# Optimization experiments

Measured on AMD Instinct MI355X. Metric: run time of the kernel, lower is better.

## Reference

```python
import jax, jax.numpy as jnp
import numpy as np

NUM_NODES = 100000
EMB = 64
HID = 128
OUT = 64
N_EDGES = 1600000
N_LABEL = 200000


def setup_inputs() -> dict:
    key = jax.random.key(0)
    ks = jax.random.split(key, 8)
    return {
        "emb": jax.random.normal(ks[0], (NUM_NODES, EMB), jnp.float32) * 0.05,
        "w1l": jax.random.normal(ks[1], (HID, EMB), jnp.float32) * 0.05,
        "w1r": jax.random.normal(ks[2], (HID, EMB), jnp.float32) * 0.05,
        "b1": jnp.zeros((HID,), jnp.float32),
        "w2l": jax.random.normal(ks[3], (OUT, HID), jnp.float32) * 0.05,
        "w2r": jax.random.normal(ks[4], (OUT, HID), jnp.float32) * 0.05,
        "b2": jnp.zeros((OUT,), jnp.float32),
        "edge_index": jax.random.randint(ks[5], (2, N_EDGES), 0, NUM_NODES, jnp.int32),
        "edge_label_index": jax.random.randint(ks[6], (2, N_LABEL), 0, NUM_NODES, jnp.int32),
    }


def reference(emb, w1l, w1r, b1, w2l, w2r, b2, edge_index, edge_label_index):
    # PyG SAGEConv (aggr='mean'): out = mean_{j in N(i)} x_j @ W_l^T + b_l + x_i @ W_r^T
    n = emb.shape[0]
    src, dst = edge_index[0], edge_index[1]
    # in-degree per destination node, clamped to avoid div-by-zero (isolated nodes -> 0 agg)
    deg = jax.ops.segment_sum(jnp.ones(src.shape, emb.dtype), dst, num_segments=n)
    inv_deg = 1.0 / jnp.maximum(deg, 1.0)

    def sage(x, wl, wr, b):
        agg = jax.ops.segment_sum(x[src], dst, num_segments=n) * inv_deg[:, None]
        return agg @ wl.T + x @ wr.T + b

    h = jax.nn.relu(sage(emb, w1l, w1r, b1))  # dropout is identity in eval mode
    z = sage(h, w2l, w2r, b2)  # [N, OUT]
    # dot-product decode over candidate pairs
    return jnp.sum(z[edge_label_index[0]] * z[edge_label_index[1]], axis=-1)
```

## Files before the change

kernel.cpp:

```cpp
#include <hip/hip_runtime.h>

#define NN   100000
#define EMB  64
#define HID  128
#define OUTD 64
#define NE   1600000
#define NL   200000
#define NBUK 782
#define CAPT 2560

#define BIN_BLOCKS  160
#define TILE        10240
#define CEMB_BLOCKS 400
#define CW_BLOCKS   32

typedef __attribute__((ext_vector_type(4))) float f32x4;
typedef __attribute__((ext_vector_type(8))) short s16x8;
typedef __attribute__((ext_vector_type(4))) unsigned short us4;
typedef __attribute__((ext_vector_type(8))) unsigned short us8;

__device__ __forceinline__ unsigned short f2bf(float f) {
    unsigned u = __float_as_uint(f);
    u += 0x7FFFu + ((u >> 16) & 1u);
    return (unsigned short)(u >> 16);
}
__device__ __forceinline__ float bf2f(unsigned short h) {
    return __uint_as_float(((unsigned)h) << 16);
}

__global__ void __launch_bounds__(512) prep_kernel(
        const int* __restrict__ src, const int* __restrict__ dst,
        int* __restrict__ gcur, int* __restrict__ tmp,
        const float* __restrict__ emb, unsigned short* __restrict__ embb,
        const float* __restrict__ w1l, const float* __restrict__ w1r,
        const float* __restrict__ w2l, const float* __restrict__ w2r,
        unsigned short* __restrict__ w1cat, unsigned short* __restrict__ w2cat) {
    const int bid = blockIdx.x;
    const int tid = threadIdx.x;

    if (bid < BIN_BLOCKS) {
        __shared__ int hist[NBUK];
        __shared__ int base[NBUK];
        const int t0  = bid * TILE;
        const int end = min(t0 + TILE, NE);

        for (int k = tid; k < NBUK; k += 512) hist[k] = 0;
        __syncthreads();

        for (int i = t0 + tid; i < end; i += 512)
            atomicAdd(&hist[__builtin_nontemporal_load(dst + i) >> 7], 1);
        __syncthreads();

        for (int k = tid; k < NBUK; k += 512) {
            int c = hist[k];
            base[k] = c ? atomicAdd(&gcur[k], c) : 0;
        }
        __syncthreads();

        for (int i = t0 + tid; i < end; i += 512) {
            int d = __builtin_nontemporal_load(dst + i);
            int s = __builtin_nontemporal_load(src + i);
            int b = d >> 7;
            int pos = atomicAdd(&base[b], 1);
            if (pos < CAPT) tmp[b * CAPT + pos] = ((d & 127) << 17) | s;
        }
    } else if (bid < BIN_BLOCKS + CEMB_BLOCKS) {
        for (int i = (bid - BIN_BLOCKS) * 512 + tid; i < NN * 16; i += CEMB_BLOCKS * 512) {
            float4 v = ((const float4*)emb)[i];
            us4 o;
            o.x = f2bf(v.x); o.y = f2bf(v.y); o.z = f2bf(v.z); o.w = f2bf(v.w);
            ((us4*)embb)[i] = o;
        }
    } else {
        int t = (bid - BIN_BLOCKS - CEMB_BLOCKS) * 512 + tid;
        if (t >= 128 * 128) return;
        int o = t >> 7, k = t & 127;
        w1cat[t] = f2bf(k < 64 ? w1l[o * 64 + k] : w1r[o * 64 + (k - 64)]);
        w2cat[t] = f2bf(o < 64 ? w2l[o * 128 + k] : w2r[(o - 64) * 128 + k]);
    }
}

template<bool L1>
__global__ void __launch_bounds__(512) agg_kernel(
        const int* __restrict__ gcur, const int* __restrict__ tmp,
        const unsigned short* __restrict__ xb,
        const unsigned short* __restrict__ hzb, const float* __restrict__ bias,
        unsigned short* __restrict__ outb) {
    __shared__ int scnt[128];
    __shared__ int soff[128];
    __shared__ int scur[128];
    __shared__ int slist[CAPT];

    const int b    = blockIdx.x;
    const int tid  = threadIdx.x;
    const int lane = tid & 63;
    const int wv   = tid >> 6;

    if (tid < 128) scnt[tid] = 0;
    __syncthreads();

    const int cnt = min(gcur[b], CAPT);
    const int* tb = tmp + b * CAPT;

    for (int i = tid; i < cnt; i += 512)
        atomicAdd(&scnt[tb[i] >> 17], 1);
    __syncthreads();

    if (tid == 0) {
        int acc = 0;
        for (int r = 0; r < 128; ++r) {
            soff[r] = acc;
            scur[r] = acc;
            acc += scnt[r];
        }
    }
    __syncthreads();

    for (int i = tid; i < cnt; i += 512) {
        int p = tb[i];
        int pos = atomicAdd(&scur[p >> 17], 1);
        slist[pos] = p & 0x1FFFF;
    }
    __syncthreads();

    const float bb = L1 ? 0.f : bias[lane];

#define LDX(c) bf2f(xb[(size_t)(c) * 64 + lane])
    for (int r = wv; r < 128; r += 8) {
        const int node = b * 128 + r;
        if (node >= NN) continue;
        const int s = soff[r];
        const int d = scnt[r];
        float acc = 0.f;
        int j = 0;
        for (; j + 8 <= d; j += 8) {
            int c0 = slist[s + j + 0], c1 = slist[s + j + 1];
            int c2 = slist[s + j + 2], c3 = slist[s + j + 3];
            int c4 = slist[s + j + 4], c5 = slist[s + j + 5];
            int c6 = slist[s + j + 6], c7 = slist[s + j + 7];
            float v0 = LDX(c0), v1 = LDX(c1), v2 = LDX(c2), v3 = LDX(c3);
            float v4 = LDX(c4), v5 = LDX(c5), v6 = LDX(c6), v7 = LDX(c7);
            acc += ((v0 + v1) + (v2 + v3)) + ((v4 + v5) + (v6 + v7));
        }
        if (j + 4 <= d) {
            int c0 = slist[s + j + 0], c1 = slist[s + j + 1];
            int c2 = slist[s + j + 2], c3 = slist[s + j + 3];
            float v0 = LDX(c0), v1 = LDX(c1), v2 = LDX(c2), v3 = LDX(c3);
            acc += (v0 + v1) + (v2 + v3);
            j += 4;
        }
        for (; j < d; ++j) acc += LDX(slist[s + j]);

        const float inv = 1.0f / fmaxf((float)d, 1.0f);
        if (L1) {
            outb[(size_t)node * 64 + lane] = f2bf(acc * inv);
        } else {
            outb[(size_t)node * 64 + lane] =
                f2bf(acc * inv + bf2f(hzb[(size_t)node * 64 + lane]) + bb);
        }
    }
#undef LDX
}

__global__ void __launch_bounds__(512) gemm_mfma_kernel(
        const unsigned short* __restrict__ aggb, const unsigned short* __restrict__ embb,
        const unsigned short* __restrict__ w1cat, const float* __restrict__ b1,
        const unsigned short* __restrict__ w2cat,
        unsigned short* __restrict__ p2b, unsigned short* __restrict__ hzb) {
    __shared__ unsigned short h_lds[128 * 136];

    const int tid  = threadIdx.x;
    const int lane = tid & 63;
    const int w    = tid >> 6;
    const int l15  = lane & 15;
    const int lk   = lane >> 4;
    const int n_base = blockIdx.x * 128;
    const int mrow0  = w * 16;

    f32x4 acc[8];
#pragma unroll
    for (int nt = 0; nt < 8; ++nt) acc[nt] = (f32x4)(0.f);

    s16x8 a[4];
    {
        const int n = n_base + mrow0 + l15;
        const bool ok = n < NN;
#pragma unroll
        for (int ks = 0; ks < 4; ++ks) {
            const int kc = ks * 32 + lk * 8;
            a[ks] = (s16x8)(short)0;
            if (ok) {
                const unsigned short* ap = (kc < 64)
                    ? (aggb + (size_t)n * 64 + kc)
                    : (embb + (size_t)n * 64 + (kc - 64));
                a[ks] = *(const s16x8*)ap;
            }
        }
    }
#pragma unroll
    for (int ks = 0; ks < 4; ++ks) {
        const int kc = ks * 32 + lk * 8;
#pragma unroll
        for (int nt = 0; nt < 8; ++nt) {
            s16x8 bv = *(const s16x8*)(w1cat + (nt * 16 + l15) * 128 + kc);
            acc[nt] = __builtin_amdgcn_mfma_f32_16x16x32_bf16(a[ks], bv, acc[nt], 0, 0, 0);
        }
    }

    float b1v[8];
#pragma unroll
    for (int nt = 0; nt < 8; ++nt) b1v[nt] = b1[nt * 16 + l15];
#pragma unroll
    for (int nt = 0; nt < 8; ++nt) {
        f32x4 d = acc[nt];
        int o = nt * 16 + l15;
        int r0 = mrow0 + lk * 4;
#pragma unroll
        for (int j = 0; j < 4; ++j)
            h_lds[(r0 + j) * 136 + o] = f2bf(fmaxf(d[j] + b1v[nt], 0.f));
    }

#pragma unroll
    for (int nt = 0; nt < 8; ++nt) acc[nt] = (f32x4)(0.f);

    s16x8 a2[4];
#pragma unroll
    for (int ks = 0; ks < 4; ++ks)
        a2[ks] = *(const s16x8*)&h_lds[(mrow0 + l15) * 136 + ks * 32 + lk * 8];
#pragma unroll
    for (int ks = 0; ks < 4; ++ks) {
        const int kc = ks * 32 + lk * 8;
#pragma unroll
        for (int nt = 0; nt < 8; ++nt) {
            s16x8 bv = *(const s16x8*)(w2cat + (nt * 16 + l15) * 128 + kc);
            acc[nt] = __builtin_amdgcn_mfma_f32_16x16x32_bf16(a2[ks], bv, acc[nt], 0, 0, 0);
        }
    }

#pragma unroll
    for (int nt = 0; nt < 8; ++nt) {
        f32x4 d = acc[nt];
        int col = nt * 16 + l15;
        int r0 = mrow0 + lk * 4;
#pragma unroll
        for (int j = 0; j < 4; ++j)
            h_lds[(r0 + j) * 136 + col] = f2bf(d[j]);
    }
    {
        const int row8 = lane >> 3;
        const int seg  = lane & 7;
#pragma unroll
        for (int half = 0; half < 2; ++half) {
            int r = mrow0 + half * 8 + row8;
            int n = n_base + r;
            us8 vp = *(const us8*)&h_lds[r * 136 + seg * 8];
            us8 vh = *(const us8*)&h_lds[r * 136 + 64 + seg * 8];
            if (n < NN) {
                *(us8*)&p2b[(size_t)n * 64 + seg * 8] = vp;
                *(us8*)&hzb[(size_t)n * 64 + seg * 8] = vh;
            }
        }
    }
}

__global__ void decode_kernel(const int* __restrict__ a, const int* __restrict__ b,
                              const unsigned short* __restrict__ zb, float* __restrict__ out) {
    int t = blockIdx.x * blockDim.x + threadIdx.x;
    int k = t >> 4;
    int q = t & 15;
    if (k >= NL) return;
    int ia = a[k], ib = b[k];
    us4 va = ((const us4*)zb)[ia * 16 + q];
    us4 vb = ((const us4*)zb)[ib * 16 + q];
    float s = bf2f(va.x) * bf2f(vb.x) + bf2f(va.y) * bf2f(vb.y)
            + bf2f(va.z) * bf2f(vb.z) + bf2f(va.w) * bf2f(vb.w);
    s += __shfl_xor(s, 1, 64);
    s += __shfl_xor(s, 2, 64);
    s += __shfl_xor(s, 4, 64);
    s += __shfl_xor(s, 8, 64);
    if (q == 0) __builtin_nontemporal_store(s, out + k);
}

extern "C" void kernel_launch(void* const* d_in, const int* in_sizes, int n_in,
                              void* d_out, int out_size, void* d_ws, size_t ws_size,
                              hipStream_t stream) {
    const float* emb = (const float*)d_in[0];
    const float* w1l = (const float*)d_in[1];
    const float* w1r = (const float*)d_in[2];
    const float* b1  = (const float*)d_in[3];
    const float* w2l = (const float*)d_in[4];
    const float* w2r = (const float*)d_in[5];
    const float* b2  = (const float*)d_in[6];
    const int*   ei  = (const int*)d_in[7];
    const int*   eli = (const int*)d_in[8];
    float* out = (float*)d_out;

    int* gcur = (int*)d_ws;
    int* tmp  = gcur + 1024;
    unsigned short* aggb  = (unsigned short*)(tmp + (size_t)NBUK * CAPT);
    unsigned short* embb  = aggb + (size_t)NN * 64;
    unsigned short* p2b   = embb + (size_t)NN * 64;
    unsigned short* zb    = p2b + (size_t)NN * 64;
    unsigned short* hzb   = zb + (size_t)NN * 64;
    unsigned short* w1cat = hzb + (size_t)NN * 64;
    unsigned short* w2cat = w1cat + 128 * 128;

    const int* src = ei;
    const int* dst = ei + NE;

    hipMemsetAsync(gcur, 0, 1024 * sizeof(int), stream);

    prep_kernel<<<BIN_BLOCKS + CEMB_BLOCKS + CW_BLOCKS, 512, 0, stream>>>(
        src, dst, gcur, tmp, emb, embb, w1l, w1r, w2l, w2r, w1cat, w2cat);

    agg_kernel<true><<<NBUK, 512, 0, stream>>>(gcur, tmp, embb, nullptr, nullptr, aggb);

    const int NT = (NN + 127) / 128;
    gemm_mfma_kernel<<<NT, 512, 0, stream>>>(aggb, embb, w1cat, b1, w2cat, p2b, hzb);

    agg_kernel<false><<<NBUK, 512, 0, stream>>>(gcur, tmp, p2b, hzb, b2, zb);

    decode_kernel<<<(NL * 16 + 255) / 256, 256, 0, stream>>>(eli, eli + NL, zb, out);
}
```

Before: 216.8 us.

## Fuse layer-1 mean aggregation with the two MFMA GEMMs in one kernel

The layer-1 neighbour aggregation and the dense MFMA GEMM stage now run in a single kernel per 128-node bucket. The aggregated rows stay in LDS instead of being written to and re-read from a global buffer, and one kernel launch is removed. Shared memory is reused between the edge list and the hidden tile, which raises LDS use per block. The final outputs are now written straight from registers with scalar bf16 stores rather than staged through LDS into vectorised stores, which may make the stores less coalesced.

```diff
diff --git a/kernel.cpp b/kernel.cpp
--- a/kernel.cpp
+++ b/kernel.cpp
@@ -1,9 +1,6 @@
 #include <hip/hip_runtime.h>
 
 #define NN   100000
-#define EMB  64
-#define HID  128
-#define OUTD 64
 #define NE   1600000
 #define NL   200000
 #define NBUK 782
@@ -17,7 +14,6 @@
 typedef __attribute__((ext_vector_type(4))) float f32x4;
 typedef __attribute__((ext_vector_type(8))) short s16x8;
 typedef __attribute__((ext_vector_type(4))) unsigned short us4;
-typedef __attribute__((ext_vector_type(8))) unsigned short us8;
 
 __device__ __forceinline__ unsigned short f2bf(float f) {
     unsigned u = __float_as_uint(f);
@@ -80,8 +76,159 @@
     }
 }
 
-template<bool L1>
-__global__ void __launch_bounds__(512) agg_kernel(
+__global__ void __launch_bounds__(512) agg1_gemm_kernel(
+        const int* __restrict__ gcur, const int* __restrict__ tmp,
+        const unsigned short* __restrict__ embb,
+        const unsigned short* __restrict__ w1cat, const float* __restrict__ b1,
+        const unsigned short* __restrict__ w2cat,
+        unsigned short* __restrict__ p2b, unsigned short* __restrict__ hzb) {
+    __shared__ __align__(16) char smem[128 * 136 * 2];
+    __shared__ unsigned short agg_lds[128 * 72];
+
+    int* scnt  = (int*)smem;
+    int* soff  = scnt + 128;
+    int* scur  = soff + 128;
+    int* slist = scur + 128;
+    unsigned short* h_lds = (unsigned short*)smem;
+
+    const int b    = blockIdx.x;
+    const int tid  = threadIdx.x;
+    const int lane = tid & 63;
+    const int wv   = tid >> 6;
+
+    if (tid < 128) scnt[tid] = 0;
+    __syncthreads();
+
+    const int cnt = min(gcur[b], CAPT);
+    const int* tb = tmp + b * CAPT;
+
+    for (int i = tid; i < cnt; i += 512)
+        atomicAdd(&scnt[tb[i] >> 17], 1);
+    __syncthreads();
+
+    if (tid == 0) {
+        int acc = 0;
+        for (int r = 0; r < 128; ++r) {
+            soff[r] = acc;
+            scur[r] = acc;
+            acc += scnt[r];
+        }
+    }
+    __syncthreads();
+
+    for (int i = tid; i < cnt; i += 512) {
+        int p = tb[i];
+        int pos = atomicAdd(&scur[p >> 17], 1);
+        slist[pos] = p & 0x1FFFF;
+    }
+    __syncthreads();
+
+#define LDX(c) bf2f(embb[(size_t)(c) * 64 + lane])
+    for (int r = wv; r < 128; r += 8) {
+        const int s = soff[r];
+        const int d = scnt[r];
+        float acc = 0.f;
+        int j = 0;
+        for (; j + 8 <= d; j += 8) {
+            int c0 = slist[s + j + 0], c1 = slist[s + j + 1];
+            int c2 = slist[s + j + 2], c3 = slist[s + j + 3];
+            int c4 = slist[s + j + 4], c5 = slist[s + j + 5];
+            int c6 = slist[s + j + 6], c7 = slist[s + j + 7];
+            float v0 = LDX(c0), v1 = LDX(c1), v2 = LDX(c2), v3 = LDX(c3);
+            float v4 = LDX(c4), v5 = LDX(c5), v6 = LDX(c6), v7 = LDX(c7);
+            acc += ((v0 + v1) + (v2 + v3)) + ((v4 + v5) + (v6 + v7));
+        }
+        if (j + 4 <= d) {
+            int c0 = slist[s + j + 0], c1 = slist[s + j + 1];
+            int c2 = slist[s + j + 2], c3 = slist[s + j + 3];
+            float v0 = LDX(c0), v1 = LDX(c1), v2 = LDX(c2), v3 = LDX(c3);
+            acc += (v0 + v1) + (v2 + v3);
+            j += 4;
+        }
+        for (; j < d; ++j) acc += LDX(slist[s + j]);
+        agg_lds[r * 72 + lane] = f2bf(acc / fmaxf((float)d, 1.0f));
+    }
+#undef LDX
+    __syncthreads();
+
+    const int l15   = lane & 15;
+    const int lk    = lane >> 4;
+    const int mrow0 = wv * 16;
+    const int n_base = b * 128;
+
+    f32x4 acc4[8];
+#pragma unroll
+    for (int nt = 0; nt < 8; ++nt) acc4[nt] = (f32x4)(0.f);
+
+    s16x8 a[4];
+    {
+        const int rr = mrow0 + l15;
+        const int n  = n_base + rr;
+        a[0] = *(const s16x8*)&agg_lds[rr * 72 + lk * 8];
+        a[1] = *(const s16x8*)&agg_lds[rr * 72 + 32 + lk * 8];
+        a[2] = (s16x8)(short)0;
+        a[3] = (s16x8)(short)0;
+        if (n < NN) {
+            a[2] = *(const s16x8*)(embb + (size_t)n * 64 + lk * 8);
+            a[3] = *(const s16x8*)(embb + (size_t)n * 64 + 32 + lk * 8);
+        }
+    }
+#pragma unroll
+    for (int ks = 0; ks < 4; ++ks) {
+        const int kc = ks * 32 + lk * 8;
+#pragma unroll
+        for (int nt = 0; nt < 8; ++nt) {
+            s16x8 bv = *(const s16x8*)(w1cat + (nt * 16 + l15) * 128 + kc);
+            acc4[nt] = __builtin_amdgcn_mfma_f32_16x16x32_bf16(a[ks], bv, acc4[nt], 0, 0, 0);
+        }
+    }
+
+    float b1v[8];
+#pragma unroll
+    for (int nt = 0; nt < 8; ++nt) b1v[nt] = b1[nt * 16 + l15];
+#pragma unroll
+    for (int nt = 0; nt < 8; ++nt) {
+        f32x4 d = acc4[nt];
+        int o = nt * 16 + l15;
+        int r0 = mrow0 + lk * 4;
+#pragma unroll
+        for (int j = 0; j < 4; ++j)
+            h_lds[(r0 + j) * 136 + o] = f2bf(fmaxf(d[j] + b1v[nt], 0.f));
+    }
+
+#pragma unroll
+    for (int nt = 0; nt < 8; ++nt) acc4[nt] = (f32x4)(0.f);
+
+    s16x8 a2[4];
+#pragma unroll
+    for (int ks = 0; ks < 4; ++ks)
+        a2[ks] = *(const s16x8*)&h_lds[(mrow0 + l15) * 136 + ks * 32 + lk * 8];
+#pragma unroll
+    for (int ks = 0; ks < 4; ++ks) {
+        const int kc = ks * 32 + lk * 8;
+#pragma unroll
+        for (int nt = 0; nt < 8; ++nt) {
+            s16x8 bv = *(const s16x8*)(w2cat + (nt * 16 + l15) * 128 + kc);
+            acc4[nt] = __builtin_amdgcn_mfma_f32_16x16x32_bf16(a2[ks], bv, acc4[nt], 0, 0, 0);
+        }
+    }
+
+#pragma unroll
+    for (int nt = 0; nt < 8; ++nt) {
+        f32x4 d = acc4[nt];
+        int col = nt * 16 + l15;
+        int r0 = n_base + mrow0 + lk * 4;
+#pragma unroll
+        for (int j = 0; j < 4; ++j) {
+            int r = r0 + j;
+            if (r >= NN) continue;
+            if (nt < 4) p2b[(size_t)r * 64 + col] = f2bf(d[j]);
+            else        hzb[(size_t)r * 64 + (col - 64)] = f2bf(d[j]);
+        }
+    }
+}
+
+__global__ void __launch_bounds__(512) agg2_kernel(
         const int* __restrict__ gcur, const int* __restrict__ tmp,
         const unsigned short* __restrict__ xb,
         const unsigned short* __restrict__ hzb, const float* __restrict__ bias,
@@ -123,7 +270,7 @@
     }
     __syncthreads();
 
-    const float bb = L1 ? 0.f : bias[lane];
+    const float bb = bias[lane];
 
 #define LDX(c) bf2f(xb[(size_t)(c) * 64 + lane])
     for (int r = wv; r < 128; r += 8) {
@@ -151,116 +298,10 @@
         }
         for (; j < d; ++j) acc += LDX(slist[s + j]);
 
-        const float inv = 1.0f / fmaxf((float)d, 1.0f);
-        if (L1) {
-            outb[(size_t)node * 64 + lane] = f2bf(acc * inv);
-        } else {
-            outb[(size_t)node * 64 + lane] =
-                f2bf(acc * inv + bf2f(hzb[(size_t)node * 64 + lane]) + bb);
-        }
+        outb[(size_t)node * 64 + lane] =
+            f2bf(acc / fmaxf((float)d, 1.0f) + bf2f(hzb[(size_t)node * 64 + lane]) + bb);
     }
 #undef LDX
-}
-
-__global__ void __launch_bounds__(512) gemm_mfma_kernel(
-        const unsigned short* __restrict__ aggb, const unsigned short* __restrict__ embb,
-        const unsigned short* __restrict__ w1cat, const float* __restrict__ b1,
-        const unsigned short* __restrict__ w2cat,
-        unsigned short* __restrict__ p2b, unsigned short* __restrict__ hzb) {
-    __shared__ unsigned short h_lds[128 * 136];
-
-    const int tid  = threadIdx.x;
-    const int lane = tid & 63;
-    const int w    = tid >> 6;
-    const int l15  = lane & 15;
-    const int lk   = lane >> 4;
-    const int n_base = blockIdx.x * 128;
-    const int mrow0  = w * 16;
-
-    f32x4 acc[8];
-#pragma unroll
-    for (int nt = 0; nt < 8; ++nt) acc[nt] = (f32x4)(0.f);
-
-    s16x8 a[4];
-    {
-        const int n = n_base + mrow0 + l15;
-        const bool ok = n < NN;
-#pragma unroll
-        for (int ks = 0; ks < 4; ++ks) {
-            const int kc = ks * 32 + lk * 8;
-            a[ks] = (s16x8)(short)0;
-            if (ok) {
-                const unsigned short* ap = (kc < 64)
-                    ? (aggb + (size_t)n * 64 + kc)
-                    : (embb + (size_t)n * 64 + (kc - 64));
-                a[ks] = *(const s16x8*)ap;
-            }
-        }
-    }
-#pragma unroll
-    for (int ks = 0; ks < 4; ++ks) {
-        const int kc = ks * 32 + lk * 8;
-#pragma unroll
-        for (int nt = 0; nt < 8; ++nt) {
-            s16x8 bv = *(const s16x8*)(w1cat + (nt * 16 + l15) * 128 + kc);
-            acc[nt] = __builtin_amdgcn_mfma_f32_16x16x32_bf16(a[ks], bv, acc[nt], 0, 0, 0);
-        }
-    }
-
-    float b1v[8];
-#pragma unroll
-    for (int nt = 0; nt < 8; ++nt) b1v[nt] = b1[nt * 16 + l15];
-#pragma unroll
-    for (int nt = 0; nt < 8; ++nt) {
-        f32x4 d = acc[nt];
-        int o = nt * 16 + l15;
-        int r0 = mrow0 + lk * 4;
-#pragma unroll
-        for (int j = 0; j < 4; ++j)
-            h_lds[(r0 + j) * 136 + o] = f2bf(fmaxf(d[j] + b1v[nt], 0.f));
-    }
-
-#pragma unroll
-    for (int nt = 0; nt < 8; ++nt) acc[nt] = (f32x4)(0.f);
-
-    s16x8 a2[4];
-#pragma unroll
-    for (int ks = 0; ks < 4; ++ks)
-        a2[ks] = *(const s16x8*)&h_lds[(mrow0 + l15) * 136 + ks * 32 + lk * 8];
-#pragma unroll
-    for (int ks = 0; ks < 4; ++ks) {
-        const int kc = ks * 32 + lk * 8;
-#pragma unroll
-        for (int nt = 0; nt < 8; ++nt) {
-            s16x8 bv = *(const s16x8*)(w2cat + (nt * 16 + l15) * 128 + kc);
-            acc[nt] = __builtin_amdgcn_mfma_f32_16x16x32_bf16(a2[ks], bv, acc[nt], 0, 0, 0);
-        }
-    }
-
-#pragma unroll
-    for (int nt = 0; nt < 8; ++nt) {
-        f32x4 d = acc[nt];
-        int col = nt * 16 + l15;
-        int r0 = mrow0 + lk * 4;
-#pragma unroll
-        for (int j = 0; j < 4; ++j)
-            h_lds[(r0 + j) * 136 + col] = f2bf(d[j]);
-    }
-    {
-        const int row8 = lane >> 3;
-        const int seg  = lane & 7;
-#pragma unroll
-        for (int half = 0; half < 2; ++half) {
-            int r = mrow0 + half * 8 + row8;
-            int n = n_base + r;
-            us8 vp = *(const us8*)&h_lds[r * 136 + seg * 8];
-            us8 vh = *(const us8*)&h_lds[r * 136 + 64 + seg * 8];
-            if (n < NN) {
-                *(us8*)&p2b[(size_t)n * 64 + seg * 8] = vp;
-                *(us8*)&hzb[(size_t)n * 64 + seg * 8] = vh;
-            }
-        }
-    }
 }
 
 __global__ void decode_kernel(const int* __restrict__ a, const int* __restrict__ b,
@@ -297,8 +338,7 @@
 
     int* gcur = (int*)d_ws;
     int* tmp  = gcur + 1024;
-    unsigned short* aggb  = (unsigned short*)(tmp + (size_t)NBUK * CAPT);
-    unsigned short* embb  = aggb + (size_t)NN * 64;
+    unsigned short* embb  = (unsigned short*)(tmp + (size_t)NBUK * CAPT);
     unsigned short* p2b   = embb + (size_t)NN * 64;
     unsigned short* zb    = p2b + (size_t)NN * 64;
     unsigned short* hzb   = zb + (size_t)NN * 64;
@@ -313,12 +353,10 @@
     prep_kernel<<<BIN_BLOCKS + CEMB_BLOCKS + CW_BLOCKS, 512, 0, stream>>>(
         src, dst, gcur, tmp, emb, embb, w1l, w1r, w2l, w2r, w1cat, w2cat);
 
-    agg_kernel<true><<<NBUK, 512, 0, stream>>>(gcur, tmp, embb, nullptr, nullptr, aggb);
-
-    const int NT = (NN + 127) / 128;
-    gemm_mfma_kernel<<<NT, 512, 0, stream>>>(aggb, embb, w1cat, b1, w2cat, p2b, hzb);
-
-    agg_kernel<false><<<NBUK, 512, 0, stream>>>(gcur, tmp, p2b, hzb, b2, zb);
+    agg1_gemm_kernel<<<NBUK, 512, 0, stream>>>(
+        gcur, tmp, embb, w1cat, b1, w2cat, p2b, hzb);
+
+    agg2_kernel<<<NBUK, 512, 0, stream>>>(gcur, tmp, p2b, hzb, b2, zb);
 
     decode_kernel<<<(NL * 16 + 255) / 256, 256, 0, stream>>>(eli, eli + NL, zb, out);
 }
```

Measured after the change: 226.5 us. 1.04x slower.
